# Kernel optimization log

Measured on AMD Instinct MI355X. Metric: run time of the kernel, lower is better.

The kernel has to match this reference:

```python
import jax, jax.numpy as jnp
import numpy as np

N = 50000
E = 800000
FEAT, COND, HID, LAT = 64, 32, 64, 32


def gcn_conv(x, W, b, src, dst, n):
    xw = x @ W  # [N, out]
    deg = jnp.zeros((n,), xw.dtype).at[dst].add(1.0) + 1.0  # in-degree + self loop
    dinv = jax.lax.rsqrt(deg)
    coef = dinv[src] * dinv[dst]  # [E]
    msg = xw[src] * coef[:, None]  # gather + scale
    agg = jax.ops.segment_sum(msg, dst, num_segments=n)
    agg = agg + xw * (1.0 / deg)[:, None]  # self-loop contribution
    return agg + b


def setup_inputs() -> dict:
    key = jax.random.key(0)
    ks = jax.random.split(key, 12)
    s = 0.05
    return {
        "feature": jax.random.normal(ks[0], (N, FEAT), jnp.float32),
        "condition": jax.random.normal(ks[1], (N, COND), jnp.float32),
        "edge_index": jax.random.randint(ks[2], (2, E), 0, N, jnp.int64),
        "enc_i2h_W": jax.random.normal(ks[3], (FEAT + COND, HID), jnp.float32) * s,
        "enc_i2h_b": jnp.zeros((HID,), jnp.float32),
        "enc_mean_W": jax.random.normal(ks[4], (HID, LAT), jnp.float32) * s,
        "enc_mean_b": jnp.zeros((LAT,), jnp.float32),
        "enc_logvar_W": jax.random.normal(ks[5], (HID, LAT), jnp.float32) * s,
        "enc_logvar_b": jnp.zeros((LAT,), jnp.float32),
        "dec_i2h_W": jax.random.normal(ks[6], (LAT + COND, HID), jnp.float32) * s,
        "dec_i2h_b": jnp.zeros((HID,), jnp.float32),
        "dec_out_W": jax.random.normal(ks[7], (HID, FEAT), jnp.float32) * s,
        "dec_out_b": jnp.zeros((FEAT,), jnp.float32),
    }


def reference(feature, condition, edge_index,
              enc_i2h_W, enc_i2h_b, enc_mean_W, enc_mean_b,
              enc_logvar_W, enc_logvar_b,
              dec_i2h_W, dec_i2h_b, dec_out_W, dec_out_b):
    src, dst = edge_index[0], edge_index[1]
    n = feature.shape[0]
    # encoder
    x = jnp.concatenate([feature, condition], axis=1)
    h = jax.nn.relu(gcn_conv(x, enc_i2h_W, enc_i2h_b, src, dst, n))
    mean = gcn_conv(h, enc_mean_W, enc_mean_b, src, dst, n)
    logvar = gcn_conv(h, enc_logvar_W, enc_logvar_b, src, dst, n)
    noise = jax.random.normal(jax.random.key(42), logvar.shape, logvar.dtype)
    z = noise * jnp.exp(0.5 * logvar) + mean
    # decoder
    xd = jnp.concatenate([z, condition], axis=1)
    hd = jax.nn.relu(gcn_conv(xd, dec_i2h_W, dec_i2h_b, src, dst, n))
    out = gcn_conv(hd, dec_out_W, dec_out_b, src, dst, n)
    return (z, mean, logvar, out)
```

## Files before the change

### kernel.cpp

```cpp
#include <hip/hip_runtime.h>
#include <hip/hip_bf16.h>
#include <hip/hip_fp16.h>
#include <math.h>

typedef _Float16 f16;
typedef __attribute__((ext_vector_type(8))) _Float16 f16x8;
typedef __attribute__((ext_vector_type(4))) float f32x4;


static __device__ __forceinline__ unsigned rotl32(unsigned x, int d) {
  return (x << d) | (x >> (32 - d));
}

static __device__ __forceinline__ void threefry_0_42(unsigned& x0, unsigned& x1) {
  const unsigned ks0 = 0u, ks1 = 42u, ks2 = 0u ^ 42u ^ 0x1BD11BDAu;
  x0 += ks0; x1 += ks1;
#define TF_R(r) { x0 += x1; x1 = rotl32(x1, (r)); x1 ^= x0; }
  TF_R(13) TF_R(15) TF_R(26) TF_R(6)
  x0 += ks1; x1 += ks2 + 1u;
  TF_R(17) TF_R(29) TF_R(16) TF_R(24)
  x0 += ks2; x1 += ks0 + 2u;
  TF_R(13) TF_R(15) TF_R(26) TF_R(6)
  x0 += ks0; x1 += ks1 + 3u;
  TF_R(17) TF_R(29) TF_R(16) TF_R(24)
  x0 += ks1; x1 += ks2 + 4u;
  TF_R(13) TF_R(15) TF_R(26) TF_R(6)
  x0 += ks2; x1 += ks0 + 5u;
#undef TF_R
}

static __device__ __forceinline__ float erfinv_f(float u) {
  float w = -logf((1.0f - u) * (1.0f + u));
  float p;
  if (w < 5.0f) {
    w = w - 2.5f;
    p = 2.81022636e-08f;
    p = fmaf(p, w, 3.43273939e-07f);
    p = fmaf(p, w, -3.5233877e-06f);
    p = fmaf(p, w, -4.39150654e-06f);
    p = fmaf(p, w, 0.00021858087f);
    p = fmaf(p, w, -0.00125372503f);
    p = fmaf(p, w, -0.00417768164f);
    p = fmaf(p, w, 0.246640727f);
    p = fmaf(p, w, 1.50140941f);
  } else {
    w = sqrtf(w) - 3.0f;
    p = -0.000200214257f;
    p = fmaf(p, w, 0.000100950558f);
    p = fmaf(p, w, 0.00134934322f);
    p = fmaf(p, w, -0.00367342844f);
    p = fmaf(p, w, 0.00573950773f);
    p = fmaf(p, w, -0.0076224613f);
    p = fmaf(p, w, 0.00943887047f);
    p = fmaf(p, w, 1.00167406f);
    p = fmaf(p, w, 2.83297682f);
  }
  return p * u;
}

static __device__ __forceinline__ float jax_normal_at(unsigned j) {
  unsigned x0 = 0u, x1 = j;
  threefry_0_42(x0, x1);
  unsigned bits = x0 ^ x1;
  float f = __uint_as_float((bits >> 9) | 0x3f800000u) - 1.0f;
  float u = fmaf(f, 1.99999994f, -0.99999994f);
  return 1.41421356237f * erfinv_f(u);
}


__global__ void zero_i_kernel(int* __restrict__ p, int n) {
  int i = blockIdx.x * blockDim.x + threadIdx.x;
  if (i < n) p[i] = 0;
}

__global__ void degree_i_kernel(const int* __restrict__ dstI, int* __restrict__ cnt, int ne) {
  int e = blockIdx.x * blockDim.x + threadIdx.x;
  if (e < ne) atomicAdd(&cnt[dstI[e]], 1);
}

__global__ __launch_bounds__(256) void scan1_kernel(const int* __restrict__ cnt,
                                                    int* __restrict__ rowptr,
                                                    int* __restrict__ bsum, int n) {
  __shared__ int s[256];
  const int t = threadIdx.x;
  const int base = blockIdx.x * 1024 + t * 4;
  int v0, v1, v2, v3;
  if (base + 3 < n) {
    int4 v = *(const int4*)(cnt + base);
    v0 = v.x; v1 = v.y; v2 = v.z; v3 = v.w;
  } else {
    v0 = (base + 0 < n) ? cnt[base + 0] : 0;
    v1 = (base + 1 < n) ? cnt[base + 1] : 0;
    v2 = (base + 2 < n) ? cnt[base + 2] : 0;
    v3 = (base + 3 < n) ? cnt[base + 3] : 0;
  }
  int tot = v0 + v1 + v2 + v3;
  s[t] = tot;
  __syncthreads();
  for (int off = 1; off < 256; off <<= 1) {
    int x = (t >= off) ? s[t - off] : 0;
    __syncthreads();
    s[t] += x;
    __syncthreads();
  }
  int excl = s[t] - tot;
  if (t == 255) bsum[blockIdx.x] = s[t];
  if (base + 0 < n) rowptr[base + 0] = excl;
  if (base + 1 < n) rowptr[base + 1] = excl + v0;
  if (base + 2 < n) rowptr[base + 2] = excl + v0 + v1;
  if (base + 3 < n) rowptr[base + 3] = excl + v0 + v1 + v2;
}

__global__ __launch_bounds__(256) void scanP_kernel(int* __restrict__ bsum,
                                                    int* __restrict__ boff,
                                                    int nb, int* __restrict__ rowptr,
                                                    int n, int ne) {
  __shared__ int s[256];
  const int t = threadIdx.x;
  int v = (t < nb) ? bsum[t] : 0;
  s[t] = v;
  __syncthreads();
  for (int off = 1; off < 256; off <<= 1) {
    int x = (t >= off) ? s[t - off] : 0;
    __syncthreads();
    s[t] += x;
    __syncthreads();
  }
  if (t < nb) boff[t] = s[t] - v;
  if (t == 0) rowptr[n] = ne;
}

__global__ void scan2_kernel(int* __restrict__ rowptr, const int* __restrict__ boff,
                             const int* __restrict__ cnt, float* __restrict__ dinv,
                             int* __restrict__ bcur, int n) {
  int i = blockIdx.x * blockDim.x + threadIdx.x;
  if (i < n) {
    int rp = rowptr[i] + boff[i >> 10];
    rowptr[i] = rp;
    if ((i & 255) == 0) bcur[i >> 8] = rp;
    float d = (float)cnt[i] + 1.0f;
    dinv[i] = 1.0f / sqrtf(d);
  }
}

#define EPB 2048
__global__ __launch_bounds__(256) void fillA_kernel(
    const int* __restrict__ srcI, const int* __restrict__ dstI,
    int* __restrict__ bcur, unsigned* __restrict__ coarse, int ne) {
  __shared__ int hist[256], hpre[256], hcur[256], gbase[256];
  __shared__ unsigned st[EPB];
  const int tid = threadIdx.x;
  const int base = blockIdx.x * EPB;

  hist[tid] = 0; hcur[tid] = 0;
  __syncthreads();

  int s[8], d[8];
#pragma unroll
  for (int k = 0; k < 8; ++k) {
    int e = base + k * 256 + tid;
    if (e < ne) { s[k] = srcI[e]; d[k] = dstI[e]; }
    else        { s[k] = -1;      d[k] = 0; }
  }
#pragma unroll
  for (int k = 0; k < 8; ++k)
    if (s[k] >= 0) atomicAdd(&hist[d[k] >> 8], 1);
  __syncthreads();

  int hv = hist[tid];
  hpre[tid] = hv;
  __syncthreads();
  for (int off = 1; off < 256; off <<= 1) {
    int x = (tid >= off) ? hpre[tid - off] : 0;
    __syncthreads();
    hpre[tid] += x;
    __syncthreads();
  }

#pragma unroll
  for (int k = 0; k < 8; ++k) {
    if (s[k] >= 0) {
      int b = d[k] >> 8;
      int pos = (hpre[b] - hist[b]) + atomicAdd(&hcur[b], 1);
      st[pos] = ((unsigned)b << 24) | ((unsigned)(d[k] & 255) << 16) | (unsigned)s[k];
    }
  }
  if (hist[tid] > 0) gbase[tid] = atomicAdd(&bcur[tid], hist[tid]);
  __syncthreads();

  int cntE = ne - base; if (cntE > EPB) cntE = EPB;
  for (int i = tid; i < cntE; i += 256) {
    unsigned v = st[i];
    int b = v >> 24;
    int excl = hpre[b] - hist[b];
    coarse[gbase[b] + (i - excl)] = v & 0x00FFFFFFu;
  }
}

__global__ __launch_bounds__(256) void fillB_kernel(
    const unsigned* __restrict__ coarse, const int* __restrict__ rowptr,
    unsigned short* __restrict__ ssrc, int n, int ne) {
  __shared__ int rcur[256];
  const int b = blockIdx.x;
  const int r0 = b << 8;
  const int tid = threadIdx.x;
  if (r0 + tid < n) rcur[tid] = rowptr[r0 + tid];
  const int e0 = rowptr[r0];
  const int e1 = (r0 + 256 <= n) ? rowptr[r0 + 256] : ne;
  __syncthreads();
  for (int e = e0 + tid; e < e1; e += 256) {
    unsigned v = coarse[e];
    int r = (v >> 16) & 255;
    int pos = atomicAdd(&rcur[r], 1);
    ssrc[pos] = (unsigned short)(v & 0xFFFFu);
  }
}

template<int IN1, int IN2, bool X1HALF, bool DUALW>
__global__ __launch_bounds__(256) void gemm_mfma_kernel(
    const void* __restrict__ X1v, const float* __restrict__ X2,
    const float* __restrict__ Wa, const float* __restrict__ Wb,
    const float* __restrict__ dinv, __half* __restrict__ Y, int n) {
  constexpr int IN = IN1 + IN2;
  constexpr int IP = IN + 8;
  __shared__ f16 xs[128 * IP];
  __shared__ f16 wt[64 * IP];

  const int tid = threadIdx.x;
  const int base = blockIdx.x * 128;

  for (int i = tid; i < IN * 64; i += 256) {
    int k = i >> 6, c = i & 63;
    float w;
    if (DUALW) w = (c < 32) ? Wa[k * 32 + c] : Wb[k * 32 + (c - 32)];
    else       w = Wa[i];
    wt[c * IP + k] = (f16)w;
  }
  if (X1HALF) {
    const __half* X1 = (const __half*)X1v;
    for (int idx = tid; idx < 128 * (IN1 / 8); idx += 256) {
      int node = idx / (IN1 / 8);
      int k8 = (idx % (IN1 / 8)) * 8;
      int g = base + node;
      f16x8 v = {};
      if (g < n) v = *(const f16x8*)(X1 + (size_t)g * IN1 + k8);
      *(f16x8*)&xs[node * IP + k8] = v;
    }
  } else {
    const float* X1 = (const float*)X1v;
    for (int idx = tid; idx < 128 * (IN1 / 4); idx += 256) {
      int node = idx / (IN1 / 4);
      int k4 = (idx % (IN1 / 4)) * 4;
      int g = base + node;
      float4 v = (g < n) ? *(const float4*)(X1 + (size_t)g * IN1 + k4)
                         : make_float4(0.f, 0.f, 0.f, 0.f);
      f16* p = &xs[node * IP + k4];
      p[0] = (f16)v.x; p[1] = (f16)v.y; p[2] = (f16)v.z; p[3] = (f16)v.w;
    }
  }
  if (IN2 > 0) {
    for (int idx = tid; idx < 128 * (IN2 / 4); idx += 256) {
      int node = idx / (IN2 / 4);
      int k4 = (idx % (IN2 / 4)) * 4;
      int g = base + node;
      float4 v = (g < n) ? *(const float4*)(X2 + (size_t)g * IN2 + k4)
                         : make_float4(0.f, 0.f, 0.f, 0.f);
      f16* p = &xs[node * IP + IN1 + k4];
      p[0] = (f16)v.x; p[1] = (f16)v.y; p[2] = (f16)v.z; p[3] = (f16)v.w;
    }
  }
  __syncthreads();

  const int wid  = tid >> 6;
  const int lane = tid & 63;
  const int l15  = lane & 15;
  const int lk8  = (lane >> 4) * 8;

  f32x4 acc[2][4] = {{{0.f,0.f,0.f,0.f}}};
  constexpr int KB = IN / 32;
#pragma unroll
  for (int kb = 0; kb < KB; ++kb) {
    const int k0 = kb * 32 + lk8;
    f16x8 a0 = *(const f16x8*)&xs[(wid * 32 +      l15) * IP + k0];
    f16x8 a1 = *(const f16x8*)&xs[(wid * 32 + 16 + l15) * IP + k0];
#pragma unroll
    for (int ct = 0; ct < 4; ++ct) {
      f16x8 b = *(const f16x8*)&wt[(ct * 16 + l15) * IP + k0];
      acc[0][ct] = __builtin_amdgcn_mfma_f32_16x16x32_f16(a0, b, acc[0][ct], 0, 0, 0);
      acc[1][ct] = __builtin_amdgcn_mfma_f32_16x16x32_f16(a1, b, acc[1][ct], 0, 0, 0);
    }
  }

#pragma unroll
  for (int rt = 0; rt < 2; ++rt) {
#pragma unroll
    for (int i = 0; i < 4; ++i) {
      int node = base + wid * 32 + rt * 16 + (lane >> 4) * 4 + i;
      if (node < n) {
        float dv = dinv[node];
#pragma unroll
        for (int ct = 0; ct < 4; ++ct) {
          Y[(size_t)node * 64 + ct * 16 + l15] = __float2half(acc[rt][ct][i] * dv);
        }
      }
    }
  }
}

template<int MODE>
__global__ __launch_bounds__(256) void gather_kernel(
    const int* __restrict__ rowptr, const unsigned short* __restrict__ ssrc,
    const __half* __restrict__ xwp, const float* __restrict__ dinv,
    const float* __restrict__ b0, const float* __restrict__ b1,
    void* __restrict__ outv, int n) {
  const int node = (blockIdx.x * 256 + threadIdx.x) >> 6;
  const int lane = threadIdx.x & 63;
  if (node >= n) return;
  const int hf = lane >> 5;
  const int cl = lane & 31;

  float2 a1, a2, a3, a4;
  a2.x = a2.y = a3.x = a3.y = a4.x = a4.y = 0.f;
  {
    float2 f = __half22float2(((const __half2*)(xwp + (size_t)node * 64))[cl]);
    a1.x = hf ? 0.f : f.x;
    a1.y = hf ? 0.f : f.y;
  }

  const int beg = rowptr[node];
  const int end = rowptr[node + 1];
  for (int cbase = beg; cbase < end; cbase += 64) {
    int m = end - cbase; if (m > 64) m = 64;
    unsigned sv = (lane < m) ? (unsigned)ssrc[cbase + lane] : 0u;
    int k = 0;
    for (; k + 7 < m; k += 8) {
      unsigned sa = __shfl(sv, k + 0 + hf, 64);
      unsigned sb = __shfl(sv, k + 2 + hf, 64);
      unsigned sc = __shfl(sv, k + 4 + hf, 64);
      unsigned sd = __shfl(sv, k + 6 + hf, 64);
      float2 fa = __half22float2(((const __half2*)(xwp + (size_t)sa * 64))[cl]);
      float2 fb = __half22float2(((const __half2*)(xwp + (size_t)sb * 64))[cl]);
      float2 fc = __half22float2(((const __half2*)(xwp + (size_t)sc * 64))[cl]);
      float2 fd = __half22float2(((const __half2*)(xwp + (size_t)sd * 64))[cl]);
      a1.x += fa.x; a1.y += fa.y;
      a2.x += fb.x; a2.y += fb.y;
      a3.x += fc.x; a3.y += fc.y;
      a4.x += fd.x; a4.y += fd.y;
    }
    for (; k + 1 < m; k += 2) {
      unsigned sa = __shfl(sv, k + hf, 64);
      float2 fa = __half22float2(((const __half2*)(xwp + (size_t)sa * 64))[cl]);
      a1.x += fa.x; a1.y += fa.y;
    }
    if (k < m) {
      unsigned sa = __shfl(sv, k, 64);
      if (hf == 0) {
        float2 fa = __half22float2(((const __half2*)(xwp + (size_t)sa * 64))[cl]);
        a1.x += fa.x; a1.y += fa.y;
      }
    }
  }
  float2 acc;
  acc.x = (a1.x + a2.x) + (a3.x + a4.x);
  acc.y = (a1.y + a2.y) + (a3.y + a4.y);
  acc.x += __shfl(acc.x, lane ^ 32, 64);
  acc.y += __shfl(acc.y, lane ^ 32, 64);
  float dv = dinv[node];
  float vx = acc.x * dv, vy = acc.y * dv;

  if (hf != 0) return;

  const int c0 = 2 * cl;
  if (MODE == 0) {
    __half* out = (__half*)outv;
    __half2 o = __floats2half2_rn(fmaxf(vx + b0[c0], 0.0f), fmaxf(vy + b0[c0 + 1], 0.0f));
    ((__half2*)(out + (size_t)node * 64))[cl] = o;
  } else if (MODE == 2) {
    float* out = (float*)outv;
    float2 o;
    o.x = vx + b0[c0];
    o.y = vy + b0[c0 + 1];
    ((float2*)(out + (size_t)node * 64))[cl] = o;
  } else {
    float* out = (float*)outv;
    float bx = (c0 < 32) ? b0[c0] : b1[c0 - 32];
    float by = (c0 + 1 < 32) ? b0[c0 + 1] : b1[c0 + 1 - 32];
    vx += bx; vy += by;
    float ox = __shfl(vx, lane + 16, 64);
    float oy = __shfl(vy, lane + 16, 64);
    const int NZ = n * 32;
    if (cl < 16) {
      int j = node * 32 + c0;
      float n0 = jax_normal_at((unsigned)j);
      float n1 = jax_normal_at((unsigned)(j + 1));
      out[j]     = fmaf(n0, expf(0.5f * ox), vx);
      out[j + 1] = fmaf(n1, expf(0.5f * oy), vy);
      out[NZ + j]     = vx;
      out[NZ + j + 1] = vy;
    } else {
      int j = node * 32 + (c0 - 32);
      out[2 * NZ + j]     = vx;
      out[2 * NZ + j + 1] = vy;
    }
  }
}


extern "C" void kernel_launch(void* const* d_in, const int* in_sizes, int n_in,
                              void* d_out, int out_size, void* d_ws, size_t ws_size,
                              hipStream_t stream) {
  const float* feat = (const float*)d_in[0];
  const float* cond = (const float*)d_in[1];
  const int*   eidx = (const int*)d_in[2];
  const float* W1  = (const float*)d_in[3];
  const float* b1  = (const float*)d_in[4];
  const float* Wm  = (const float*)d_in[5];
  const float* bm  = (const float*)d_in[6];
  const float* Wlv = (const float*)d_in[7];
  const float* blv = (const float*)d_in[8];
  const float* Wd  = (const float*)d_in[9];
  const float* bd  = (const float*)d_in[10];
  const float* Wo  = (const float*)d_in[11];
  const float* bo  = (const float*)d_in[12];

  const int n  = in_sizes[0] / 64;
  const int ne = in_sizes[2] / 2;
  const int* srcI = eidx;
  const int* dstI = eidx + ne;
  const int nbuck = (n + 255) >> 8;

  int*   cnt    = (int*)d_ws;
  int*   rowptr = cnt + n;
  int*   bsum   = rowptr + n + 1;
  int*   boff   = bsum + 256;
  int*   bcur   = boff + 256;
  float* dinv   = (float*)(bcur + 256 + 3);
  __half* xwp   = (__half*)(dinv + n);
  __half* h     = xwp + (size_t)n * 64;
  unsigned short* ssrc = (unsigned short*)(h + (size_t)n * 64);
  unsigned* coarse = (unsigned*)(ssrc + ne + (ne & 1));

  float* dout   = (float*)d_out;
  float* zbuf   = dout;
  float* outbuf = dout + (size_t)3 * n * 32;

  const int BT = 256;
  auto blk = [](long long t) { return (int)((t + 255) / 256); };
  const int nb_n  = blk(n);
  const int nb_e  = blk(ne);
  const int nb_sc = (n + 1023) / 1024;
  const int nb_gw = blk((long long)n * 64);
  const int nb_g  = (n + 127) / 128;
  const int nb_fa = (ne + EPB - 1) / EPB;

  hipLaunchKernelGGL(zero_i_kernel, dim3(nb_n), dim3(BT), 0, stream, cnt, n);
  hipLaunchKernelGGL(degree_i_kernel, dim3(nb_e), dim3(BT), 0, stream, dstI, cnt, ne);
  hipLaunchKernelGGL(scan1_kernel, dim3(nb_sc), dim3(BT), 0, stream, cnt, rowptr, bsum, n);
  hipLaunchKernelGGL(scanP_kernel, dim3(1), dim3(BT), 0, stream, bsum, boff, nb_sc, rowptr, n, ne);
  hipLaunchKernelGGL(scan2_kernel, dim3(nb_n), dim3(BT), 0, stream, rowptr, boff, cnt, dinv, bcur, n);
  hipLaunchKernelGGL(fillA_kernel, dim3(nb_fa), dim3(BT), 0, stream, srcI, dstI, bcur, coarse, ne);
  hipLaunchKernelGGL(fillB_kernel, dim3(nbuck), dim3(BT), 0, stream, coarse, rowptr, ssrc, n, ne);

  hipLaunchKernelGGL((gemm_mfma_kernel<64, 32, false, false>), dim3(nb_g), dim3(BT), 0, stream,
                     feat, cond, W1, nullptr, dinv, xwp, n);
  hipLaunchKernelGGL((gather_kernel<0>), dim3(nb_gw), dim3(BT), 0, stream,
                     rowptr, ssrc, xwp, dinv, b1, nullptr, h, n);

  hipLaunchKernelGGL((gemm_mfma_kernel<64, 0, true, true>), dim3(nb_g), dim3(BT), 0, stream,
                     h, nullptr, Wm, Wlv, dinv, xwp, n);
  hipLaunchKernelGGL((gather_kernel<1>), dim3(nb_gw), dim3(BT), 0, stream,
                     rowptr, ssrc, xwp, dinv, bm, blv, dout, n);

  hipLaunchKernelGGL((gemm_mfma_kernel<32, 32, false, false>), dim3(nb_g), dim3(BT), 0, stream,
                     zbuf, cond, Wd, nullptr, dinv, xwp, n);
  hipLaunchKernelGGL((gather_kernel<0>), dim3(nb_gw), dim3(BT), 0, stream,
                     rowptr, ssrc, xwp, dinv, bd, nullptr, h, n);

  hipLaunchKernelGGL((gemm_mfma_kernel<64, 0, true, false>), dim3(nb_g), dim3(BT), 0, stream,
                     h, nullptr, Wo, nullptr, dinv, xwp, n);
  hipLaunchKernelGGL((gather_kernel<2>), dim3(nb_gw), dim3(BT), 0, stream,
                     rowptr, ssrc, xwp, dinv, bo, nullptr, outbuf, n);
}
```

Baseline: 232.8 us.

## Split gather tables into two 32-column halves for cache-resident aggregation

The GEMM now writes its 64-wide output as two separate 32-column fp16 tables, and each aggregation runs as two passes, one per half, with 4 edges processed in parallel per wavefront. Each half-table is half the size of the full table, so random source-row gathers are more likely to hit L2/LLC. The cost is twice as many gather launches and re-reading the CSR indices. The fused mean/logvar/z epilogue is split so the logvar pass reads back the mean written by the first pass.

```diff
diff --git a/kernel.cpp b/kernel.cpp
--- a/kernel.cpp
+++ b/kernel.cpp
@@ -220,7 +220,7 @@
 __global__ __launch_bounds__(256) void gemm_mfma_kernel(
     const void* __restrict__ X1v, const float* __restrict__ X2,
     const float* __restrict__ Wa, const float* __restrict__ Wb,
-    const float* __restrict__ dinv, __half* __restrict__ Y, int n) {
+    const float* __restrict__ dinv, __half* __restrict__ YA, __half* __restrict__ YB, int n) {
   constexpr int IN = IN1 + IN2;
   constexpr int IP = IN + 8;
   __shared__ f16 xs[128 * IP];
@@ -298,33 +298,32 @@
       int node = base + wid * 32 + rt * 16 + (lane >> 4) * 4 + i;
       if (node < n) {
         float dv = dinv[node];
-#pragma unroll
-        for (int ct = 0; ct < 4; ++ct) {
-          Y[(size_t)node * 64 + ct * 16 + l15] = __float2half(acc[rt][ct][i] * dv);
-        }
+        YA[(size_t)node * 32 +  0 + l15] = __float2half(acc[rt][0][i] * dv);
+        YA[(size_t)node * 32 + 16 + l15] = __float2half(acc[rt][1][i] * dv);
+        YB[(size_t)node * 32 +  0 + l15] = __float2half(acc[rt][2][i] * dv);
+        YB[(size_t)node * 32 + 16 + l15] = __float2half(acc[rt][3][i] * dv);
       }
     }
   }
 }
 
-template<int MODE>
-__global__ __launch_bounds__(256) void gather_kernel(
+template<int MODE, int HALF>
+__global__ __launch_bounds__(256) void gatherH_kernel(
     const int* __restrict__ rowptr, const unsigned short* __restrict__ ssrc,
-    const __half* __restrict__ xwp, const float* __restrict__ dinv,
-    const float* __restrict__ b0, const float* __restrict__ b1,
-    void* __restrict__ outv, int n) {
+    const __half* __restrict__ tbl, const float* __restrict__ dinv,
+    const float* __restrict__ bias, float* __restrict__ dout,
+    __half* __restrict__ hout, int n) {
   const int node = (blockIdx.x * 256 + threadIdx.x) >> 6;
   const int lane = threadIdx.x & 63;
   if (node >= n) return;
-  const int hf = lane >> 5;
-  const int cl = lane & 31;
-
-  float2 a1, a2, a3, a4;
-  a2.x = a2.y = a3.x = a3.y = a4.x = a4.y = 0.f;
-  {
-    float2 f = __half22float2(((const __half2*)(xwp + (size_t)node * 64))[cl]);
-    a1.x = hf ? 0.f : f.x;
-    a1.y = hf ? 0.f : f.y;
+  const int p  = lane >> 4;
+  const int cl = lane & 15;
+
+  float2 a0, a1;
+  a0.x = a0.y = a1.x = a1.y = 0.f;
+  if (p == 0) {
+    float2 f = __half22float2(((const __half2*)(tbl + (size_t)node * 32))[cl]);
+    a0 = f;
   }
 
   const int beg = rowptr[node];
@@ -332,76 +331,64 @@
   for (int cbase = beg; cbase < end; cbase += 64) {
     int m = end - cbase; if (m > 64) m = 64;
     unsigned sv = (lane < m) ? (unsigned)ssrc[cbase + lane] : 0u;
-    int k = 0;
-    for (; k + 7 < m; k += 8) {
-      unsigned sa = __shfl(sv, k + 0 + hf, 64);
-      unsigned sb = __shfl(sv, k + 2 + hf, 64);
-      unsigned sc = __shfl(sv, k + 4 + hf, 64);
-      unsigned sd = __shfl(sv, k + 6 + hf, 64);
-      float2 fa = __half22float2(((const __half2*)(xwp + (size_t)sa * 64))[cl]);
-      float2 fb = __half22float2(((const __half2*)(xwp + (size_t)sb * 64))[cl]);
-      float2 fc = __half22float2(((const __half2*)(xwp + (size_t)sc * 64))[cl]);
-      float2 fd = __half22float2(((const __half2*)(xwp + (size_t)sd * 64))[cl]);
-      a1.x += fa.x; a1.y += fa.y;
-      a2.x += fb.x; a2.y += fb.y;
-      a3.x += fc.x; a3.y += fc.y;
-      a4.x += fd.x; a4.y += fd.y;
-    }
-    for (; k + 1 < m; k += 2) {
-      unsigned sa = __shfl(sv, k + hf, 64);
-      float2 fa = __half22float2(((const __half2*)(xwp + (size_t)sa * 64))[cl]);
-      a1.x += fa.x; a1.y += fa.y;
-    }
-    if (k < m) {
-      unsigned sa = __shfl(sv, k, 64);
-      if (hf == 0) {
-        float2 fa = __half22float2(((const __half2*)(xwp + (size_t)sa * 64))[cl]);
-        a1.x += fa.x; a1.y += fa.y;
+    const int body = m & ~7;
+    for (int k = 0; k < body; k += 8) {
+      unsigned s0 = __shfl(sv, k + p, 64);
+      unsigned s1 = __shfl(sv, k + 4 + p, 64);
+      float2 f0 = __half22float2(((const __half2*)(tbl + (size_t)s0 * 32))[cl]);
+      float2 f1 = __half22float2(((const __half2*)(tbl + (size_t)s1 * 32))[cl]);
+      a0.x += f0.x; a0.y += f0.y;
+      a1.x += f1.x; a1.y += f1.y;
+    }
+    {
+      int k = body;
+      unsigned s0 = __shfl(sv, k + p, 64);
+      unsigned s1 = __shfl(sv, (k + 4 + p) & 63, 64);
+      if (k + p < m) {
+        float2 f0 = __half22float2(((const __half2*)(tbl + (size_t)s0 * 32))[cl]);
+        a0.x += f0.x; a0.y += f0.y;
       }
+      if (k + 4 + p < m) {
+        float2 f1 = __half22float2(((const __half2*)(tbl + (size_t)s1 * 32))[cl]);
+        a1.x += f1.x; a1.y += f1.y;
+      }
     }
   }
   float2 acc;
-  acc.x = (a1.x + a2.x) + (a3.x + a4.x);
-  acc.y = (a1.y + a2.y) + (a3.y + a4.y);
+  acc.x = a0.x + a1.x;
+  acc.y = a0.y + a1.y;
+  acc.x += __shfl(acc.x, lane ^ 16, 64);
+  acc.y += __shfl(acc.y, lane ^ 16, 64);
   acc.x += __shfl(acc.x, lane ^ 32, 64);
   acc.y += __shfl(acc.y, lane ^ 32, 64);
-  float dv = dinv[node];
-  float vx = acc.x * dv, vy = acc.y * dv;
-
-  if (hf != 0) return;
-
-  const int c0 = 2 * cl;
+  const float dv = dinv[node];
+  float vx = acc.x * dv + bias[2 * cl];
+  float vy = acc.y * dv + bias[2 * cl + 1];
+
+  if (p != 0) return;
+
   if (MODE == 0) {
-    __half* out = (__half*)outv;
-    __half2 o = __floats2half2_rn(fmaxf(vx + b0[c0], 0.0f), fmaxf(vy + b0[c0 + 1], 0.0f));
-    ((__half2*)(out + (size_t)node * 64))[cl] = o;
+    __half2 o = __floats2half2_rn(fmaxf(vx, 0.0f), fmaxf(vy, 0.0f));
+    ((__half2*)(hout + (size_t)node * 64 + HALF * 32))[cl] = o;
   } else if (MODE == 2) {
-    float* out = (float*)outv;
-    float2 o;
-    o.x = vx + b0[c0];
-    o.y = vy + b0[c0 + 1];
-    ((float2*)(out + (size_t)node * 64))[cl] = o;
+    float2 o; o.x = vx; o.y = vy;
+    ((float2*)(dout + (size_t)node * 64 + HALF * 32))[cl] = o;
+  } else if (MODE == 1 && HALF == 0) {
+    const int NZ = n * 32;
+    float2 o; o.x = vx; o.y = vy;
+    ((float2*)(dout + NZ + (size_t)node * 32))[cl] = o;
   } else {
-    float* out = (float*)outv;
-    float bx = (c0 < 32) ? b0[c0] : b1[c0 - 32];
-    float by = (c0 + 1 < 32) ? b0[c0 + 1] : b1[c0 + 1 - 32];
-    vx += bx; vy += by;
-    float ox = __shfl(vx, lane + 16, 64);
-    float oy = __shfl(vy, lane + 16, 64);
     const int NZ = n * 32;
-    if (cl < 16) {
-      int j = node * 32 + c0;
-      float n0 = jax_normal_at((unsigned)j);
-      float n1 = jax_normal_at((unsigned)(j + 1));
-      out[j]     = fmaf(n0, expf(0.5f * ox), vx);
-      out[j + 1] = fmaf(n1, expf(0.5f * oy), vy);
-      out[NZ + j]     = vx;
-      out[NZ + j + 1] = vy;
-    } else {
-      int j = node * 32 + (c0 - 32);
-      out[2 * NZ + j]     = vx;
-      out[2 * NZ + j + 1] = vy;
-    }
+    float2 o; o.x = vx; o.y = vy;
+    ((float2*)(dout + 2 * NZ + (size_t)node * 32))[cl] = o;
+    float2 mv = ((const float2*)(dout + NZ + (size_t)node * 32))[cl];
+    int j = node * 32 + 2 * cl;
+    float n0 = jax_normal_at((unsigned)j);
+    float n1 = jax_normal_at((unsigned)(j + 1));
+    float2 z;
+    z.x = fmaf(n0, expf(0.5f * vx), mv.x);
+    z.y = fmaf(n1, expf(0.5f * vy), mv.y);
+    ((float2*)(dout + (size_t)node * 32))[cl] = z;
   }
 }
 
@@ -435,8 +422,9 @@
   int*   boff   = bsum + 256;
   int*   bcur   = boff + 256;
   float* dinv   = (float*)(bcur + 256 + 3);
-  __half* xwp   = (__half*)(dinv + n);
-  __half* h     = xwp + (size_t)n * 64;
+  __half* xwA   = (__half*)(dinv + n);
+  __half* xwB   = xwA + (size_t)n * 32;
+  __half* h     = xwB + (size_t)n * 32;
   unsigned short* ssrc = (unsigned short*)(h + (size_t)n * 64);
   unsigned* coarse = (unsigned*)(ssrc + ne + (ne & 1));
 
@@ -462,22 +450,30 @@
   hipLaunchKernelGGL(fillB_kernel, dim3(nbuck), dim3(BT), 0, stream, coarse, rowptr, ssrc, n, ne);
 
   hipLaunchKernelGGL((gemm_mfma_kernel<64, 32, false, false>), dim3(nb_g), dim3(BT), 0, stream,
-                     feat, cond, W1, nullptr, dinv, xwp, n);
-  hipLaunchKernelGGL((gather_kernel<0>), dim3(nb_gw), dim3(BT), 0, stream,
-                     rowptr, ssrc, xwp, dinv, b1, nullptr, h, n);
+                     feat, cond, W1, nullptr, dinv, xwA, xwB, n);
+  hipLaunchKernelGGL((gatherH_kernel<0, 0>), dim3(nb_gw), dim3(BT), 0, stream,
+                     rowptr, ssrc, xwA, dinv, b1, nullptr, h, n);
+  hipLaunchKernelGGL((gatherH_kernel<0, 1>), dim3(nb_gw), dim3(BT), 0, stream,
+                     rowptr, ssrc, xwB, dinv, b1 + 32, nullptr, h, n);
 
   hipLaunchKernelGGL((gemm_mfma_kernel<64, 0, true, true>), dim3(nb_g), dim3(BT), 0, stream,
-                     h, nullptr, Wm, Wlv, dinv, xwp, n);
-  hipLaunchKernelGGL((gather_kernel<1>), dim3(nb_gw), dim3(BT), 0, stream,
-                     rowptr, ssrc, xwp, dinv, bm, blv, dout, n);
+                     h, nullptr, Wm, Wlv, dinv, xwA, xwB, n);
+  hipLaunchKernelGGL((gatherH_kernel<1, 0>), dim3(nb_gw), dim3(BT), 0, stream,
+                     rowptr, ssrc, xwA, dinv, bm, dout, nullptr, n);
+  hipLaunchKernelGGL((gatherH_kernel<1, 1>), dim3(nb_gw), dim3(BT), 0, stream,
+                     rowptr, ssrc, xwB, dinv, blv, dout, nullptr, n);
 
   hipLaunchKernelGGL((gemm_mfma_kernel<32, 32, false, false>), dim3(nb_g), dim3(BT), 0, stream,
-                     zbuf, cond, Wd, nullptr, dinv, xwp, n);
-  hipLaunchKernelGGL((gather_kernel<0>), dim3(nb_gw), dim3(BT), 0, stream,
-                     rowptr, ssrc, xwp, dinv, bd, nullptr, h, n);
+                     zbuf, cond, Wd, nullptr, dinv, xwA, xwB, n);
+  hipLaunchKernelGGL((gatherH_kernel<0, 0>), dim3(nb_gw), dim3(BT), 0, stream,
+                     rowptr, ssrc, xwA, dinv, bd, nullptr, h, n);
+  hipLaunchKernelGGL((gatherH_kernel<0, 1>), dim3(nb_gw), dim3(BT), 0, stream,
+                     rowptr, ssrc, xwB, dinv, bd + 32, nullptr, h, n);
 
   hipLaunchKernelGGL((gemm_mfma_kernel<64, 0, true, false>), dim3(nb_g), dim3(BT), 0, stream,
-                     h, nullptr, Wo, nullptr, dinv, xwp, n);
-  hipLaunchKernelGGL((gather_kernel<2>), dim3(nb_gw), dim3(BT), 0, stream,
-                     rowptr, ssrc, xwp, dinv, bo, nullptr, outbuf, n);
-}
+                     h, nullptr, Wo, nullptr, dinv, xwA, xwB, n);
+  hipLaunchKernelGGL((gatherH_kernel<2, 0>), dim3(nb_gw), dim3(BT), 0, stream,
+                     rowptr, ssrc, xwA, dinv, bo, outbuf, nullptr, n);
+  hipLaunchKernelGGL((gatherH_kernel<2, 1>), dim3(nb_gw), dim3(BT), 0, stream,
+                     rowptr, ssrc, xwB, dinv, bo + 32, outbuf, nullptr, n);
+}
```

Result: slower. 291.9 us (+25.4%).
